# Optimization experiments

Hardware: AMD Instinct MI355X
Metric: run time of the kernel (lower is better)

Reference implementation:

```python
import jax, jax.numpy as jnp
import numpy as np

N = 500_000      # nodes
E = 1_500_000    # edges (avg degree ~3, AIG-like)
F_IN = 4         # node feature dim
H = 32           # hidden dim fixed by module
S = 7            # state feature dim
BN_EPS = 1e-5


def setup_inputs():
    key = jax.random.key(0)
    ks = jax.random.split(key, 32)
    rn = lambda k, shape, s=0.1: jax.random.normal(k, shape, dtype=jnp.float32) * s
    inp = {}
    inp["states"] = rn(ks[0], (S,), 1.0)
    inp["x"] = rn(ks[1], (N, F_IN), 1.0)
    inp["edge_index"] = jax.random.randint(ks[2], (2, E), 0, N, dtype=jnp.int32)
    inp["edge_attr"] = rn(ks[3], (E, 1), 1.0)
    inp["batch"] = jnp.zeros((N,), dtype=jnp.int32)  # single graph
    dims = [F_IN, H, H]
    for i, (d, k0) in enumerate(zip(dims, [4, 10, 16]), start=1):
        inp[f"eps{i}"] = jnp.zeros((1,), jnp.float32)
        inp[f"elw{i}"] = rn(ks[k0], (d,))            # edge lin: Linear(1, d)
        inp[f"elb{i}"] = jnp.zeros((d,), jnp.float32)
        inp[f"w{i}"] = rn(ks[k0 + 1], (d, H))
        inp[f"b{i}"] = jnp.zeros((H,), jnp.float32)
        inp[f"g{i}"] = jnp.ones((H,), jnp.float32)   # BN gamma
        inp[f"bt{i}"] = jnp.zeros((H,), jnp.float32) # BN beta
    inp["sw"] = rn(ks[22], (S, 16))
    inp["sb"] = jnp.zeros((16,), jnp.float32)
    inp["a1w"] = rn(ks[23], (H + 16, H))
    inp["a1b"] = jnp.zeros((H,), jnp.float32)
    inp["a2w"] = rn(ks[24], (H, 6))
    inp["a2b"] = jnp.zeros((6,), jnp.float32)
    return inp


def _bn(h, g, b):
    # BatchNorm1d over node dim (training-mode batch statistics)
    mu = h.mean(0)
    var = h.var(0)
    return (h - mu) * jax.lax.rsqrt(var + BN_EPS) * g + b


def _gine(x, src, dst, edge_attr, eps, elw, elb, w, b, g, bt):
    # GINEConv: nn((1+eps)*x_i + sum_j relu(x_j + lin(e_ij)))
    e = edge_attr * elw[None, :] + elb                  # [E, d]
    m = jax.nn.relu(x[src] + e)                          # gather + edge-add + relu
    agg = jax.ops.segment_sum(m, dst, num_segments=x.shape[0])  # scatter-sum
    h = (1.0 + eps) * x + agg
    return jax.nn.relu(_bn(h @ w + b, g, bt))


def reference(states, x, edge_index, edge_attr, batch,
              eps1, elw1, elb1, w1, b1, g1, bt1,
              eps2, elw2, elb2, w2, b2, g2, bt2,
              eps3, elw3, elb3, w3, b3, g3, bt3,
              sw, sb, a1w, a1b, a2w, a2b):
    src, dst = edge_index[0], edge_index[1]
    h = _gine(x, src, dst, edge_attr, eps1, elw1, elb1, w1, b1, g1, bt1)
    h = _gine(h, src, dst, edge_attr, eps2, elw2, elb2, w2, b2, g2, bt2)
    h = _gine(h, src, dst, edge_attr, eps3, elw3, elb3, w3, b3, g3, bt3)
    # (global mean/max pooling in the torch forward only feeds the cached
    #  value-head input, not the returned actor output -> omitted here)
    state_x = jax.nn.relu(states @ sw + sb)              # [16]
    a = jnp.concatenate([h, jnp.broadcast_to(state_x, (h.shape[0], 16))], axis=1)
    a = jax.nn.relu(a @ a1w + a1b)
    logits = a @ a2w + a2b                               # [N, num_actions]
    return jax.nn.softmax(logits, axis=-1)               # global_softmax=False
```

## Files before the change

kernel.cpp:

```cpp
#include <hip/hip_runtime.h>
#include <hip/hip_fp16.h>
#include <math.h>

#define TPB 256
#define SCAN_CHUNK 1024
#define NBLK_LAYER 2048
#define NGROUPS (NBLK_LAYER * 8)

struct alignas(16) half8 { __half h[8]; };

__global__ __launch_bounds__(256) void prep_kernel(
    const float* __restrict__ states, const float* __restrict__ sw,
    const float* __restrict__ sb, const float* __restrict__ a1w,
    const float* __restrict__ a1b, float* __restrict__ stats,
    float* __restrict__ c2, int zcount) {
  int t = threadIdx.x;
  for (int j = t; j < zcount; j += 256) stats[j] = 0.0f;
  __shared__ float sx[16];
  if (t < 16) {
    float acc = sb[t];
#pragma unroll
    for (int k = 0; k < 7; ++k) acc += states[k] * sw[k * 16 + t];
    sx[t] = fmaxf(acc, 0.0f);
  }
  __syncthreads();
  if (t < 32) {
    float acc = a1b[t];
#pragma unroll
    for (int k = 0; k < 16; ++k) acc += sx[k] * a1w[(32 + k) * 32 + t];
    c2[t] = acc;
  }
}

__global__ __launch_bounds__(256) void hist_k(const int* __restrict__ dst,
                                              int* __restrict__ cnt, int E) {
  int e = blockIdx.x * TPB + threadIdx.x;
  if (e >= E) return;
  atomicAdd(&cnt[dst[e]], 1);
}

__global__ __launch_bounds__(256) void scan1_k(const int* __restrict__ cnt,
                                               int* __restrict__ pre,
                                               int* __restrict__ bsum, int N) {
  __shared__ int lds[256];
  int b = blockIdx.x, t = threadIdx.x;
  int base = b * SCAN_CHUNK + t * 4;
  int c0 = (base + 0 < N) ? cnt[base + 0] : 0;
  int c1 = (base + 1 < N) ? cnt[base + 1] : 0;
  int c2 = (base + 2 < N) ? cnt[base + 2] : 0;
  int c3 = (base + 3 < N) ? cnt[base + 3] : 0;
  int s = c0 + c1 + c2 + c3;
  lds[t] = s;
  __syncthreads();
  int val = s;
  for (int off = 1; off < 256; off <<= 1) {
    int add = (t >= off) ? lds[t - off] : 0;
    __syncthreads();
    val += add;
    lds[t] = val;
    __syncthreads();
  }
  int excl = val - s;
  if (base + 0 < N) pre[base + 0] = excl;
  if (base + 1 < N) pre[base + 1] = excl + c0;
  if (base + 2 < N) pre[base + 2] = excl + c0 + c1;
  if (base + 3 < N) pre[base + 3] = excl + c0 + c1 + c2;
  if (t == 255) bsum[b] = val;
}

__global__ __launch_bounds__(512) void scan2_k(int* __restrict__ bsum, int nb) {
  __shared__ int lds[512];
  int t = threadIdx.x;
  int v = (t < nb) ? bsum[t] : 0;
  lds[t] = v;
  __syncthreads();
  int val = v;
  for (int off = 1; off < 512; off <<= 1) {
    int add = (t >= off) ? lds[t - off] : 0;
    __syncthreads();
    val += add;
    lds[t] = val;
    __syncthreads();
  }
  if (t < nb) bsum[t] = val - v;
}

__global__ __launch_bounds__(256) void scan3_k(int* __restrict__ pre,
                                               int* __restrict__ cursor,
                                               const int* __restrict__ bsum,
                                               int N, int E) {
  int i = blockIdx.x * TPB + threadIdx.x;
  if (i == 0) pre[N] = E;
  if (i >= N) return;
  int v = pre[i] + bsum[i >> 10];
  pre[i] = v;
  cursor[i] = v;
}

__global__ __launch_bounds__(256) void scatter2_k(
    const int* __restrict__ src, const int* __restrict__ dst,
    const float* __restrict__ ea, int* __restrict__ cursor,
    int2* __restrict__ pe, int E) {
  int e = blockIdx.x * TPB + threadIdx.x;
  if (e >= E) return;
  int p = atomicAdd(&cursor[dst[e]], 1);
  pe[p] = make_int2(src[e], __float_as_int(ea[e]));
}

__global__ __launch_bounds__(256) void layer1_k(
    const int* __restrict__ rowptr, const int2* __restrict__ pe,
    const float* __restrict__ x, const float* __restrict__ elw,
    const float* __restrict__ elb, const float* __restrict__ w,
    const float* __restrict__ b, const float* __restrict__ epsp,
    float* __restrict__ z, float* __restrict__ ostats, int N) {
  const int tid = threadIdx.x;
  const int c = tid & 31;
  const int group0 = blockIdx.x * 8 + (tid >> 5);
  float wc0 = w[0 * 32 + c], wc1 = w[1 * 32 + c], wc2 = w[2 * 32 + c],
        wc3 = w[3 * 32 + c];
  float bc = b[c];
  float w0 = elw[0], w1 = elw[1], w2 = elw[2], w3 = elw[3];
  float e0 = elb[0], e1 = elb[1], e2 = elb[2], e3 = elb[3];
  float one_eps = 1.0f + epsp[0];
  float sl = 0.f, sq = 0.f;
  for (int i = group0; i < N; i += NGROUPS) {
    int p0 = rowptr[i], p1 = rowptr[i + 1];
    float a0 = 0.f, a1 = 0.f, a2 = 0.f, a3 = 0.f;
    for (int p = p0 + c; p < p1; p += 32) {
      int2 e = pe[p];
      float a = __int_as_float(e.y);
      float4 xv = *reinterpret_cast<const float4*>(x + (size_t)e.x * 4);
      a0 += fmaxf(xv.x + fmaf(a, w0, e0), 0.f);
      a1 += fmaxf(xv.y + fmaf(a, w1, e1), 0.f);
      a2 += fmaxf(xv.z + fmaf(a, w2, e2), 0.f);
      a3 += fmaxf(xv.w + fmaf(a, w3, e3), 0.f);
    }
#pragma unroll
    for (int off = 16; off; off >>= 1) {
      a0 += __shfl_xor(a0, off, 32);
      a1 += __shfl_xor(a1, off, 32);
      a2 += __shfl_xor(a2, off, 32);
      a3 += __shfl_xor(a3, off, 32);
    }
    float4 xv = *reinterpret_cast<const float4*>(x + (size_t)i * 4);
    float h0 = fmaf(one_eps, xv.x, a0);
    float h1 = fmaf(one_eps, xv.y, a1);
    float h2 = fmaf(one_eps, xv.z, a2);
    float h3 = fmaf(one_eps, xv.w, a3);
    float zv = bc;
    zv = fmaf(h0, wc0, zv);
    zv = fmaf(h1, wc1, zv);
    zv = fmaf(h2, wc2, zv);
    zv = fmaf(h3, wc3, zv);
    z[(size_t)i * 32 + c] = zv;
    sl += zv;
    sq = fmaf(zv, zv, sq);
  }
  __shared__ float rs[256], rq[256];
  rs[tid] = sl;
  rq[tid] = sq;
  __syncthreads();
  if (tid < 32) {
    float a = 0.f, qq = 0.f;
#pragma unroll
    for (int g = 0; g < 8; ++g) {
      a += rs[g * 32 + tid];
      qq += rq[g * 32 + tid];
    }
    int slot = blockIdx.x & 7;
    atomicAdd(&ostats[slot * 32 + tid], a);
    atomicAdd(&ostats[256 + slot * 32 + tid], qq);
  }
}

__global__ __launch_bounds__(256) void fin_k(
    const float* __restrict__ z, const float* __restrict__ pstats,
    const float* __restrict__ g, const float* __restrict__ bt,
    __half* __restrict__ h16, int N) {
  __shared__ float sscale[32], sshift[32];
  if (threadIdx.x < 32) {
    int c = threadIdx.x;
    float ps = 0.f, pq = 0.f;
#pragma unroll
    for (int s = 0; s < 8; ++s) {
      ps += pstats[s * 32 + c];
      pq += pstats[256 + s * 32 + c];
    }
    float mu = ps / (float)N;
    float var = pq / (float)N - mu * mu;
    float sc = rsqrtf(var + 1e-5f) * g[c];
    sscale[c] = sc;
    sshift[c] = bt[c] - mu * sc;
  }
  __syncthreads();
  long long t = (long long)blockIdx.x * 256 + threadIdx.x;
  if (t >= (long long)N * 4) return;
  size_t base = (size_t)t * 8;
  int c0 = (int)(base & 31);
  float4 z0 = *reinterpret_cast<const float4*>(z + base);
  float4 z1 = *reinterpret_cast<const float4*>(z + base + 4);
  half8 o;
  o.h[0] = __float2half(fmaxf(fmaf(sscale[c0 + 0], z0.x, sshift[c0 + 0]), 0.f));
  o.h[1] = __float2half(fmaxf(fmaf(sscale[c0 + 1], z0.y, sshift[c0 + 1]), 0.f));
  o.h[2] = __float2half(fmaxf(fmaf(sscale[c0 + 2], z0.z, sshift[c0 + 2]), 0.f));
  o.h[3] = __float2half(fmaxf(fmaf(sscale[c0 + 3], z0.w, sshift[c0 + 3]), 0.f));
  o.h[4] = __float2half(fmaxf(fmaf(sscale[c0 + 4], z1.x, sshift[c0 + 4]), 0.f));
  o.h[5] = __float2half(fmaxf(fmaf(sscale[c0 + 5], z1.y, sshift[c0 + 5]), 0.f));
  o.h[6] = __float2half(fmaxf(fmaf(sscale[c0 + 6], z1.z, sshift[c0 + 6]), 0.f));
  o.h[7] = __float2half(fmaxf(fmaf(sscale[c0 + 7], z1.w, sshift[c0 + 7]), 0.f));
  *reinterpret_cast<half8*>(h16 + base) = o;
}

__global__ __launch_bounds__(256) void layerH_k(
    const int* __restrict__ rowptr, const int2* __restrict__ pe,
    const __half* __restrict__ h16, const float* __restrict__ elw,
    const float* __restrict__ elb, const float* __restrict__ w,
    const float* __restrict__ b, const float* __restrict__ epsp,
    float* __restrict__ z, float* __restrict__ ostats, int N) {
  const int tid = threadIdx.x;
  const int c = tid & 31;
  const int gib = tid >> 5;
  const int group0 = blockIdx.x * 8 + gib;
  float wcol[32];
#pragma unroll
  for (int k = 0; k < 32; ++k) wcol[k] = w[k * 32 + c];
  float elwc = elw[c], elbc = elb[c], bc = b[c];
  float one_eps = 1.0f + epsp[0];
  float sl = 0.f, sq = 0.f;
  __shared__ float hlds[256];
  for (int i = group0; i < N; i += NGROUPS) {
    int p0 = rowptr[i], p1 = rowptr[i + 1];
    float hself = __half2float(h16[(size_t)i * 32 + c]);
    float acc = 0.f;
    for (int p = p0; p < p1; ++p) {
      int2 e = pe[p];
      float hs = __half2float(h16[(size_t)e.x * 32 + c]);
      acc += fmaxf(hs + fmaf(__int_as_float(e.y), elwc, elbc), 0.f);
    }
    float hh = fmaf(one_eps, hself, acc);
    hlds[tid] = hh;
    float zv = bc;
    const float4* hp = reinterpret_cast<const float4*>(&hlds[gib * 32]);
#pragma unroll
    for (int kk = 0; kk < 8; ++kk) {
      float4 h4 = hp[kk];
      zv = fmaf(h4.x, wcol[kk * 4 + 0], zv);
      zv = fmaf(h4.y, wcol[kk * 4 + 1], zv);
      zv = fmaf(h4.z, wcol[kk * 4 + 2], zv);
      zv = fmaf(h4.w, wcol[kk * 4 + 3], zv);
    }
    z[(size_t)i * 32 + c] = zv;
    sl += zv;
    sq = fmaf(zv, zv, sq);
  }
  __shared__ float rs[256], rq[256];
  rs[tid] = sl;
  rq[tid] = sq;
  __syncthreads();
  if (tid < 32) {
    float a = 0.f, qq = 0.f;
#pragma unroll
    for (int g = 0; g < 8; ++g) {
      a += rs[g * 32 + tid];
      qq += rq[g * 32 + tid];
    }
    int slot = blockIdx.x & 7;
    atomicAdd(&ostats[slot * 32 + tid], a);
    atomicAdd(&ostats[256 + slot * 32 + tid], qq);
  }
}

__global__ __launch_bounds__(256) void head_k(
    const float* __restrict__ z, const float* __restrict__ pstats,
    const float* __restrict__ pg, const float* __restrict__ pbt,
    const float* __restrict__ a1w, const float* __restrict__ c2,
    const float* __restrict__ a2w, const float* __restrict__ a2b,
    float* __restrict__ out, int N) {
  const int tid = threadIdx.x;
  const int c = tid & 31;
  const int gib = tid >> 5;
  const int group0 = blockIdx.x * 8 + gib;
  float ps = 0.f, pq = 0.f;
#pragma unroll
  for (int s = 0; s < 8; ++s) {
    ps += pstats[s * 32 + c];
    pq += pstats[256 + s * 32 + c];
  }
  float mu = ps / (float)N;
  float var = pq / (float)N - mu * mu;
  float scale = rsqrtf(var + 1e-5f) * pg[c];
  float shift = pbt[c] - mu * scale;
  float wcol[32];
#pragma unroll
  for (int k = 0; k < 32; ++k) wcol[k] = a1w[k * 32 + c];
  float c2c = c2[c];
  float ar0 = a2w[c * 6 + 0], ar1 = a2w[c * 6 + 1], ar2 = a2w[c * 6 + 2],
        ar3 = a2w[c * 6 + 3], ar4 = a2w[c * 6 + 4], ar5 = a2w[c * 6 + 5];
  float b0 = a2b[0], b1 = a2b[1], b2 = a2b[2], b3 = a2b[3], b4 = a2b[4],
        b5 = a2b[5];
  __shared__ float ylds[256];
  for (int i = group0; i < N; i += NGROUPS) {
    float y = fmaxf(fmaf(scale, z[(size_t)i * 32 + c], shift), 0.f);
    ylds[tid] = y;
    float a1 = c2c;
    const float4* yp = reinterpret_cast<const float4*>(&ylds[gib * 32]);
#pragma unroll
    for (int kk = 0; kk < 8; ++kk) {
      float4 y4 = yp[kk];
      a1 = fmaf(y4.x, wcol[kk * 4 + 0], a1);
      a1 = fmaf(y4.y, wcol[kk * 4 + 1], a1);
      a1 = fmaf(y4.z, wcol[kk * 4 + 2], a1);
      a1 = fmaf(y4.w, wcol[kk * 4 + 3], a1);
    }
    a1 = fmaxf(a1, 0.f);
    float l0 = a1 * ar0, l1 = a1 * ar1, l2 = a1 * ar2, l3 = a1 * ar3,
          l4 = a1 * ar4, l5 = a1 * ar5;
#pragma unroll
    for (int off = 16; off; off >>= 1) {
      l0 += __shfl_xor(l0, off, 32);
      l1 += __shfl_xor(l1, off, 32);
      l2 += __shfl_xor(l2, off, 32);
      l3 += __shfl_xor(l3, off, 32);
      l4 += __shfl_xor(l4, off, 32);
      l5 += __shfl_xor(l5, off, 32);
    }
    l0 += b0; l1 += b1; l2 += b2; l3 += b3; l4 += b4; l5 += b5;
    float mx = fmaxf(fmaxf(fmaxf(l0, l1), fmaxf(l2, l3)), fmaxf(l4, l5));
    float e0s = __expf(l0 - mx), e1s = __expf(l1 - mx), e2s = __expf(l2 - mx),
          e3s = __expf(l3 - mx), e4s = __expf(l4 - mx), e5s = __expf(l5 - mx);
    float inv = 1.0f / (e0s + e1s + e2s + e3s + e4s + e5s);
    float v = e0s;
    v = (c == 1) ? e1s : v;
    v = (c == 2) ? e2s : v;
    v = (c == 3) ? e3s : v;
    v = (c == 4) ? e4s : v;
    v = (c == 5) ? e5s : v;
    if (c < 6) out[(size_t)i * 6 + c] = v * inv;
  }
}

__global__ __launch_bounds__(256) void edge_d4(
    const int* __restrict__ src, const int* __restrict__ dst,
    const float* __restrict__ ea, const float* __restrict__ x,
    const float* __restrict__ elw, const float* __restrict__ elb,
    float* __restrict__ agg, int E) {
  int e = blockIdx.x * TPB + threadIdx.x;
  if (e >= E) return;
  int s = src[e], d = dst[e];
  float a = ea[e];
  float4 xv = *reinterpret_cast<const float4*>(x + (size_t)s * 4);
  float m0 = fmaxf(xv.x + a * elw[0] + elb[0], 0.0f);
  float m1 = fmaxf(xv.y + a * elw[1] + elb[1], 0.0f);
  float m2 = fmaxf(xv.z + a * elw[2] + elb[2], 0.0f);
  float m3 = fmaxf(xv.w + a * elw[3] + elb[3], 0.0f);
  float* ap = agg + (size_t)d * 32;
  atomicAdd(ap + 0, m0);
  atomicAdd(ap + 1, m1);
  atomicAdd(ap + 2, m2);
  atomicAdd(ap + 3, m3);
}

__global__ __launch_bounds__(256) void edge_d32(
    const int* __restrict__ src, const int* __restrict__ dst,
    const float* __restrict__ ea, const float* __restrict__ x,
    const float* __restrict__ elw, const float* __restrict__ elb,
    float* __restrict__ agg, int E) {
  int tid = blockIdx.x * TPB + threadIdx.x;
  int e = tid >> 5;
  int c = tid & 31;
  if (e >= E) return;
  int s = src[e], d = dst[e];
  float a = ea[e];
  float m = fmaxf(x[(size_t)s * 32 + c] + a * elw[c] + elb[c], 0.0f);
  atomicAdd(agg + (size_t)d * 32 + c, m);
}

template <int DIN>
__global__ __launch_bounds__(256) void node_a(
    const float* __restrict__ x, float* aggz, const float* __restrict__ w,
    const float* __restrict__ b, const float* __restrict__ epsp,
    float* __restrict__ ssum, float* __restrict__ ssq, int N) {
  int i = blockIdx.x * TPB + threadIdx.x;
  float zv[32];
  if (i < N) {
    float one_eps = 1.0f + epsp[0];
    float h[DIN];
    if constexpr (DIN == 4) {
      float4 xv = *reinterpret_cast<const float4*>(x + (size_t)i * 4);
      float4 av = *reinterpret_cast<const float4*>(aggz + (size_t)i * 32);
      h[0] = one_eps * xv.x + av.x;
      h[1] = one_eps * xv.y + av.y;
      h[2] = one_eps * xv.z + av.z;
      h[3] = one_eps * xv.w + av.w;
    } else {
#pragma unroll
      for (int k0 = 0; k0 < 32; k0 += 4) {
        float4 xv = *reinterpret_cast<const float4*>(x + (size_t)i * 32 + k0);
        float4 av =
            *reinterpret_cast<const float4*>(aggz + (size_t)i * 32 + k0);
        h[k0 + 0] = one_eps * xv.x + av.x;
        h[k0 + 1] = one_eps * xv.y + av.y;
        h[k0 + 2] = one_eps * xv.z + av.z;
        h[k0 + 3] = one_eps * xv.w + av.w;
      }
    }
#pragma unroll
    for (int c = 0; c < 32; ++c) zv[c] = b[c];
#pragma unroll
    for (int k = 0; k < DIN; ++k)
#pragma unroll
      for (int c = 0; c < 32; ++c) zv[c] = fmaf(h[k], w[k * 32 + c], zv[c]);
#pragma unroll
    for (int c0 = 0; c0 < 32; c0 += 4) {
      float4 o = make_float4(zv[c0], zv[c0 + 1], zv[c0 + 2], zv[c0 + 3]);
      *reinterpret_cast<float4*>(aggz + (size_t)i * 32 + c0) = o;
    }
  } else {
#pragma unroll
    for (int c = 0; c < 32; ++c) zv[c] = 0.0f;
  }
  __shared__ float ls[32], lq[32];
  if (threadIdx.x < 32) {
    ls[threadIdx.x] = 0.0f;
    lq[threadIdx.x] = 0.0f;
  }
  __syncthreads();
#pragma unroll
  for (int c = 0; c < 32; ++c) {
    float v = zv[c];
    float q = zv[c] * zv[c];
#pragma unroll
    for (int off = 32; off > 0; off >>= 1) {
      v += __shfl_xor(v, off, 64);
      q += __shfl_xor(q, off, 64);
    }
    if ((threadIdx.x & 63) == 0) {
      atomicAdd(&ls[c], v);
      atomicAdd(&lq[c], q);
    }
  }
  __syncthreads();
  if (threadIdx.x < 32) {
    atomicAdd(&ssum[threadIdx.x], ls[threadIdx.x]);
    atomicAdd(&ssq[threadIdx.x], lq[threadIdx.x]);
  }
}

__global__ __launch_bounds__(256) void node_b(
    const float* __restrict__ z, const float* __restrict__ ssum,
    const float* __restrict__ ssq, const float* __restrict__ g,
    const float* __restrict__ bt, float* __restrict__ out, int N) {
  __shared__ float sscale[32], sshift[32];
  if (threadIdx.x < 32) {
    int c = threadIdx.x;
    float mu = ssum[c] / (float)N;
    float var = ssq[c] / (float)N - mu * mu;
    float inv = 1.0f / sqrtf(var + 1e-5f);
    float sc = inv * g[c];
    sscale[c] = sc;
    sshift[c] = bt[c] - mu * sc;
  }
  __syncthreads();
  int i = blockIdx.x * TPB + threadIdx.x;
  if (i >= N) return;
#pragma unroll
  for (int c0 = 0; c0 < 32; c0 += 4) {
    float4 zv = *reinterpret_cast<const float4*>(z + (size_t)i * 32 + c0);
    float4 o;
    o.x = fmaxf(zv.x * sscale[c0 + 0] + sshift[c0 + 0], 0.0f);
    o.y = fmaxf(zv.y * sscale[c0 + 1] + sshift[c0 + 1], 0.0f);
    o.z = fmaxf(zv.z * sscale[c0 + 2] + sshift[c0 + 2], 0.0f);
    o.w = fmaxf(zv.w * sscale[c0 + 3] + sshift[c0 + 3], 0.0f);
    *reinterpret_cast<float4*>(out + (size_t)i * 32 + c0) = o;
  }
}

__global__ __launch_bounds__(256) void node_b3_head(
    const float* __restrict__ z, const float* __restrict__ ssum,
    const float* __restrict__ ssq, const float* __restrict__ g,
    const float* __restrict__ bt, const float* __restrict__ a1w,
    const float* __restrict__ c2, const float* __restrict__ a2w,
    const float* __restrict__ a2b, float* __restrict__ out, int N) {
  __shared__ float sscale[32], sshift[32];
  if (threadIdx.x < 32) {
    int c = threadIdx.x;
    float mu = ssum[c] / (float)N;
    float var = ssq[c] / (float)N - mu * mu;
    float inv = 1.0f / sqrtf(var + 1e-5f);
    float sc = inv * g[c];
    sscale[c] = sc;
    sshift[c] = bt[c] - mu * sc;
  }
  __syncthreads();
  int i = blockIdx.x * TPB + threadIdx.x;
  if (i >= N) return;
  float y[32];
#pragma unroll
  for (int c0 = 0; c0 < 32; c0 += 4) {
    float4 zv = *reinterpret_cast<const float4*>(z + (size_t)i * 32 + c0);
    y[c0 + 0] = fmaxf(zv.x * sscale[c0 + 0] + sshift[c0 + 0], 0.0f);
    y[c0 + 1] = fmaxf(zv.y * sscale[c0 + 1] + sshift[c0 + 1], 0.0f);
    y[c0 + 2] = fmaxf(zv.z * sscale[c0 + 2] + sshift[c0 + 2], 0.0f);
    y[c0 + 3] = fmaxf(zv.w * sscale[c0 + 3] + sshift[c0 + 3], 0.0f);
  }
  float a1[32];
#pragma unroll
  for (int c = 0; c < 32; ++c) a1[c] = c2[c];
#pragma unroll
  for (int k = 0; k < 32; ++k)
#pragma unroll
    for (int c = 0; c < 32; ++c) a1[c] = fmaf(y[k], a1w[k * 32 + c], a1[c]);
#pragma unroll
  for (int c = 0; c < 32; ++c) a1[c] = fmaxf(a1[c], 0.0f);
  float lg[6];
#pragma unroll
  for (int j = 0; j < 6; ++j) lg[j] = a2b[j];
#pragma unroll
  for (int k = 0; k < 32; ++k)
#pragma unroll
    for (int j = 0; j < 6; ++j) lg[j] = fmaf(a1[k], a2w[k * 6 + j], lg[j]);
  float mx = lg[0];
#pragma unroll
  for (int j = 1; j < 6; ++j) mx = fmaxf(mx, lg[j]);
  float s = 0.0f;
#pragma unroll
  for (int j = 0; j < 6; ++j) {
    lg[j] = expf(lg[j] - mx);
    s += lg[j];
  }
  float rs = 1.0f / s;
#pragma unroll
  for (int j = 0; j < 6; ++j) out[(size_t)i * 6 + j] = lg[j] * rs;
}

extern "C" void kernel_launch(void* const* d_in, const int* in_sizes, int n_in,
                              void* d_out, int out_size, void* d_ws,
                              size_t ws_size, hipStream_t stream) {
  const float* states = (const float*)d_in[0];
  const float* x = (const float*)d_in[1];
  const int* ei = (const int*)d_in[2];
  const float* ea = (const float*)d_in[3];
  const float* eps1 = (const float*)d_in[5];
  const float* elw1 = (const float*)d_in[6];
  const float* elb1 = (const float*)d_in[7];
  const float* w1 = (const float*)d_in[8];
  const float* b1 = (const float*)d_in[9];
  const float* g1 = (const float*)d_in[10];
  const float* bt1 = (const float*)d_in[11];
  const float* eps2 = (const float*)d_in[12];
  const float* elw2 = (const float*)d_in[13];
  const float* elb2 = (const float*)d_in[14];
  const float* w2 = (const float*)d_in[15];
  const float* b2 = (const float*)d_in[16];
  const float* g2 = (const float*)d_in[17];
  const float* bt2 = (const float*)d_in[18];
  const float* eps3 = (const float*)d_in[19];
  const float* elw3 = (const float*)d_in[20];
  const float* elb3 = (const float*)d_in[21];
  const float* w3 = (const float*)d_in[22];
  const float* b3 = (const float*)d_in[23];
  const float* g3 = (const float*)d_in[24];
  const float* bt3 = (const float*)d_in[25];
  const float* sw = (const float*)d_in[26];
  const float* sb = (const float*)d_in[27];
  const float* a1w = (const float*)d_in[28];
  const float* a1b = (const float*)d_in[29];
  const float* a2w = (const float*)d_in[30];
  const float* a2b = (const float*)d_in[31];

  int N = in_sizes[1] / 4;
  int E = in_sizes[3];
  const int* src = ei;
  const int* dst = ei + E;
  float* out = (float*)d_out;

  float* zA = (float*)d_ws;
  float* stats = zA + (size_t)N * 32;
  float* c2csr = stats + 1536;
  __half* h16 = (__half*)(c2csr + 32);
  int* peBase = (int*)(c2csr + 32 + (size_t)N * 16);
  int* rowptr = peBase + (size_t)2 * E;
  int* cursor = rowptr + (N + 1);
  int* bsum = cursor + N;
  int2* pe = (int2*)peBase;

  int nblkN = (N + TPB - 1) / TPB;
  int nblkE = (E + TPB - 1) / TPB;
  int nblkFin = (int)(((long long)N * 4 + TPB - 1) / TPB);
  int nb = (N + SCAN_CHUNK - 1) / SCAN_CHUNK;

  size_t need =
      ((size_t)48 * N + 1568 + (size_t)2 * E + (size_t)2 * N + 1 + 512 + 8) * 4;

  if (ws_size >= need && nb <= 512) {
    prep_kernel<<<1, TPB, 0, stream>>>(states, sw, sb, a1w, a1b, stats, c2csr,
                                       1536);
    hipMemsetAsync(cursor, 0, (size_t)N * sizeof(int), stream);
    hist_k<<<nblkE, TPB, 0, stream>>>(dst, cursor, E);
    scan1_k<<<nb, TPB, 0, stream>>>(cursor, rowptr, bsum, N);
    scan2_k<<<1, 512, 0, stream>>>(bsum, nb);
    scan3_k<<<nblkN, TPB, 0, stream>>>(rowptr, cursor, bsum, N, E);
    scatter2_k<<<nblkE, TPB, 0, stream>>>(src, dst, ea, cursor, pe, E);

    layer1_k<<<NBLK_LAYER, TPB, 0, stream>>>(rowptr, pe, x, elw1, elb1, w1, b1,
                                             eps1, zA, stats + 0, N);
    fin_k<<<nblkFin, TPB, 0, stream>>>(zA, stats + 0, g1, bt1, h16, N);
    layerH_k<<<NBLK_LAYER, TPB, 0, stream>>>(rowptr, pe, h16, elw2, elb2, w2,
                                             b2, eps2, zA, stats + 512, N);
    fin_k<<<nblkFin, TPB, 0, stream>>>(zA, stats + 512, g2, bt2, h16, N);
    layerH_k<<<NBLK_LAYER, TPB, 0, stream>>>(rowptr, pe, h16, elw3, elb3, w3,
                                             b3, eps3, zA, stats + 1024, N);
    head_k<<<NBLK_LAYER, TPB, 0, stream>>>(zA, stats + 1024, g3, bt3, a1w,
                                           c2csr, a2w, a2b, out, N);
  } else {
    float* zB = zA + (size_t)N * 32;
    float* statsFB = zB + (size_t)N * 32;
    float* c2fb = statsFB + 192;
    prep_kernel<<<1, TPB, 0, stream>>>(states, sw, sb, a1w, a1b, statsFB, c2fb,
                                       192);
    size_t aggBytes = (size_t)N * 32 * sizeof(float);
    int nblkE32 = (int)(((long long)E * 32 + TPB - 1) / TPB);
    hipMemsetAsync(zA, 0, aggBytes, stream);
    edge_d4<<<nblkE, TPB, 0, stream>>>(src, dst, ea, x, elw1, elb1, zA, E);
    node_a<4><<<nblkN, TPB, 0, stream>>>(x, zA, w1, b1, eps1, statsFB + 0,
                                         statsFB + 32, N);
    node_b<<<nblkN, TPB, 0, stream>>>(zA, statsFB + 0, statsFB + 32, g1, bt1,
                                      zB, N);
    hipMemsetAsync(zA, 0, aggBytes, stream);
    edge_d32<<<nblkE32, TPB, 0, stream>>>(src, dst, ea, zB, elw2, elb2, zA, E);
    node_a<32><<<nblkN, TPB, 0, stream>>>(zB, zA, w2, b2, eps2, statsFB + 64,
                                          statsFB + 96, N);
    node_b<<<nblkN, TPB, 0, stream>>>(zA, statsFB + 64, statsFB + 96, g2, bt2,
                                      zB, N);
    hipMemsetAsync(zA, 0, aggBytes, stream);
    edge_d32<<<nblkE32, TPB, 0, stream>>>(src, dst, ea, zB, elw3, elb3, zA, E);
    node_a<32><<<nblkN, TPB, 0, stream>>>(zB, zA, w3, b3, eps3, statsFB + 128,
                                          statsFB + 160, N);
    node_b3_head<<<nblkN, TPB, 0, stream>>>(zA, statsFB + 128, statsFB + 160,
                                            g3, bt3, a1w, c2fb, a2w, a2b, out,
                                            N);
  }
}
```

Before: 599.8 us.

## Partition CSR build atomics by destination range and split head logits across lanes

The histogram and scatter kernels now use 8 teams of blocks. Each team scans all edges but only does atomics for destinations in its eighth of the node range, so the atomic traffic for a team lands in a smaller region that fits better in cache, likely per XCD on MI355X given blockIdx interleaving. The cost is that each team rereads the whole dst array, eight reads in total. The head kernel also replaces the 6 parallel shuffle reductions with an LDS-staged scheme where each lane computes a partial dot product for one logit, which needs fewer shuffles and a small extra LDS round-trip.

```diff
diff --git a/kernel.cpp b/kernel.cpp
--- a/kernel.cpp
+++ b/kernel.cpp
@@ -6,6 +6,7 @@
 #define SCAN_CHUNK 1024
 #define NBLK_LAYER 2048
 #define NGROUPS (NBLK_LAYER * 8)
+#define NBLK_TEAM 2048
 
 struct alignas(16) half8 { __half h[8]; };
 
@@ -32,11 +33,19 @@
   }
 }
 
-__global__ __launch_bounds__(256) void hist_k(const int* __restrict__ dst,
-                                              int* __restrict__ cnt, int E) {
-  int e = blockIdx.x * TPB + threadIdx.x;
-  if (e >= E) return;
-  atomicAdd(&cnt[dst[e]], 1);
+__global__ __launch_bounds__(256) void hist3_k(const int* __restrict__ dst,
+                                               int* __restrict__ cnt, int E,
+                                               int N) {
+  int team = blockIdx.x & 7;
+  int member = blockIdx.x >> 3;
+  int n8 = (N + 7) >> 3;
+  int lo = team * n8;
+  int hi = lo + n8 < N ? lo + n8 : N;
+  int stride = (NBLK_TEAM >> 3) * TPB;
+  for (int e = member * TPB + threadIdx.x; e < E; e += stride) {
+    int d = dst[e];
+    if (d >= lo && d < hi) atomicAdd(&cnt[d], 1);
+  }
 }
 
 __global__ __launch_bounds__(256) void scan1_k(const int* __restrict__ cnt,
@@ -97,14 +106,23 @@
   cursor[i] = v;
 }
 
-__global__ __launch_bounds__(256) void scatter2_k(
+__global__ __launch_bounds__(256) void scatter3_k(
     const int* __restrict__ src, const int* __restrict__ dst,
     const float* __restrict__ ea, int* __restrict__ cursor,
-    int2* __restrict__ pe, int E) {
-  int e = blockIdx.x * TPB + threadIdx.x;
-  if (e >= E) return;
-  int p = atomicAdd(&cursor[dst[e]], 1);
-  pe[p] = make_int2(src[e], __float_as_int(ea[e]));
+    int2* __restrict__ pe, int E, int N) {
+  int team = blockIdx.x & 7;
+  int member = blockIdx.x >> 3;
+  int n8 = (N + 7) >> 3;
+  int lo = team * n8;
+  int hi = lo + n8 < N ? lo + n8 : N;
+  int stride = (NBLK_TEAM >> 3) * TPB;
+  for (int e = member * TPB + threadIdx.x; e < E; e += stride) {
+    int d = dst[e];
+    if (d >= lo && d < hi) {
+      int p = atomicAdd(&cursor[d], 1);
+      pe[p] = make_int2(src[e], __float_as_int(ea[e]));
+    }
+  }
 }
 
 __global__ __launch_bounds__(256) void layer1_k(
@@ -294,11 +312,16 @@
 #pragma unroll
   for (int k = 0; k < 32; ++k) wcol[k] = a1w[k * 32 + c];
   float c2c = c2[c];
-  float ar0 = a2w[c * 6 + 0], ar1 = a2w[c * 6 + 1], ar2 = a2w[c * 6 + 2],
-        ar3 = a2w[c * 6 + 3], ar4 = a2w[c * 6 + 4], ar5 = a2w[c * 6 + 5];
-  float b0 = a2b[0], b1 = a2b[1], b2 = a2b[2], b3 = a2b[3], b4 = a2b[4],
-        b5 = a2b[5];
+  const int j = c & 7;
+  const int g = c >> 3;
+  float w2r[8];
+#pragma unroll
+  for (int u = 0; u < 8; ++u)
+    w2r[u] = (j < 6) ? a2w[(8 * g + u) * 6 + j] : 0.f;
+  float bj = (j < 6) ? a2b[j] : 0.f;
   __shared__ float ylds[256];
+  __shared__ float alds[256];
+  __shared__ float llds[64];
   for (int i = group0; i < N; i += NGROUPS) {
     float y = fmaxf(fmaf(scale, z[(size_t)i * 32 + c], shift), 0.f);
     ylds[tid] = y;
@@ -313,29 +336,41 @@
       a1 = fmaf(y4.w, wcol[kk * 4 + 3], a1);
     }
     a1 = fmaxf(a1, 0.f);
-    float l0 = a1 * ar0, l1 = a1 * ar1, l2 = a1 * ar2, l3 = a1 * ar3,
-          l4 = a1 * ar4, l5 = a1 * ar5;
-#pragma unroll
-    for (int off = 16; off; off >>= 1) {
-      l0 += __shfl_xor(l0, off, 32);
-      l1 += __shfl_xor(l1, off, 32);
-      l2 += __shfl_xor(l2, off, 32);
-      l3 += __shfl_xor(l3, off, 32);
-      l4 += __shfl_xor(l4, off, 32);
-      l5 += __shfl_xor(l5, off, 32);
-    }
-    l0 += b0; l1 += b1; l2 += b2; l3 += b3; l4 += b4; l5 += b5;
-    float mx = fmaxf(fmaxf(fmaxf(l0, l1), fmaxf(l2, l3)), fmaxf(l4, l5));
-    float e0s = __expf(l0 - mx), e1s = __expf(l1 - mx), e2s = __expf(l2 - mx),
-          e3s = __expf(l3 - mx), e4s = __expf(l4 - mx), e5s = __expf(l5 - mx);
-    float inv = 1.0f / (e0s + e1s + e2s + e3s + e4s + e5s);
-    float v = e0s;
-    v = (c == 1) ? e1s : v;
-    v = (c == 2) ? e2s : v;
-    v = (c == 3) ? e3s : v;
-    v = (c == 4) ? e4s : v;
-    v = (c == 5) ? e5s : v;
-    if (c < 6) out[(size_t)i * 6 + c] = v * inv;
+    alds[tid] = a1;
+    const float4* ap =
+        reinterpret_cast<const float4*>(&alds[gib * 32 + g * 8]);
+    float4 a4a = ap[0];
+    float4 a4b = ap[1];
+    float l = a4a.x * w2r[0];
+    l = fmaf(a4a.y, w2r[1], l);
+    l = fmaf(a4a.z, w2r[2], l);
+    l = fmaf(a4a.w, w2r[3], l);
+    l = fmaf(a4b.x, w2r[4], l);
+    l = fmaf(a4b.y, w2r[5], l);
+    l = fmaf(a4b.z, w2r[6], l);
+    l = fmaf(a4b.w, w2r[7], l);
+    l += __shfl_xor(l, 8, 32);
+    l += __shfl_xor(l, 16, 32);
+    l += bj;
+    llds[gib * 8 + j] = l;
+    const float4* lp = reinterpret_cast<const float4*>(&llds[gib * 8]);
+    float4 L0 = lp[0];
+    float4 L1 = lp[1];
+    float mx =
+        fmaxf(fmaxf(fmaxf(L0.x, L0.y), fmaxf(L0.z, L0.w)), fmaxf(L1.x, L1.y));
+    float e0 = __expf(L0.x - mx), e1 = __expf(L0.y - mx),
+          e2 = __expf(L0.z - mx), e3 = __expf(L0.w - mx),
+          e4 = __expf(L1.x - mx), e5 = __expf(L1.y - mx);
+    float inv = 1.0f / (e0 + e1 + e2 + e3 + e4 + e5);
+    if (c < 6) {
+      float v = e0;
+      v = (c == 1) ? e1 : v;
+      v = (c == 2) ? e2 : v;
+      v = (c == 3) ? e3 : v;
+      v = (c == 4) ? e4 : v;
+      v = (c == 5) ? e5 : v;
+      out[(size_t)i * 6 + c] = v * inv;
+    }
   }
 }
 
@@ -596,11 +631,11 @@
     prep_kernel<<<1, TPB, 0, stream>>>(states, sw, sb, a1w, a1b, stats, c2csr,
                                        1536);
     hipMemsetAsync(cursor, 0, (size_t)N * sizeof(int), stream);
-    hist_k<<<nblkE, TPB, 0, stream>>>(dst, cursor, E);
+    hist3_k<<<NBLK_TEAM, TPB, 0, stream>>>(dst, cursor, E, N);
     scan1_k<<<nb, TPB, 0, stream>>>(cursor, rowptr, bsum, N);
     scan2_k<<<1, 512, 0, stream>>>(bsum, nb);
     scan3_k<<<nblkN, TPB, 0, stream>>>(rowptr, cursor, bsum, N, E);
-    scatter2_k<<<nblkE, TPB, 0, stream>>>(src, dst, ea, cursor, pe, E);
+    scatter3_k<<<NBLK_TEAM, TPB, 0, stream>>>(src, dst, ea, cursor, pe, E, N);
 
     layer1_k<<<NBLK_LAYER, TPB, 0, stream>>>(rowptr, pe, x, elw1, elb1, w1, b1,
                                              eps1, zA, stats + 0, N);
```

Measured after the change: 515.3 us. 1.16x faster.
